# Performance work log

Hardware: AMD Instinct MI355X
Metric: run time of the kernel (lower is better)

Reference implementation:

```python
import jax, jax.numpy as jnp
import numpy as np

B, T, D = 2, 4096, 512
H = 8  # heads; head_dim = D // H = 64


def setup_inputs() -> dict:
    key = jax.random.key(0)
    ks = jax.random.split(key, 8)
    s = 0.02
    return {
        "queries": jax.random.normal(ks[0], (B, T, D), jnp.float32),
        "keys": jax.random.normal(ks[1], (B, T, D), jnp.float32),
        "values": jax.random.normal(ks[2], (B, T, D), jnp.float32),
        "Wq": jax.random.normal(ks[3], (D, D), jnp.float32) * s,
        "Wk": jax.random.normal(ks[4], (D, D), jnp.float32) * s,
        "Wv": jax.random.normal(ks[5], (D, D), jnp.float32) * s,
        "Wo": jax.random.normal(ks[6], (D, D), jnp.float32) * s,
        "bo": jnp.zeros((D,), jnp.float32),
    }


def reference(queries, keys, values, Wq, Wk, Wv, Wo, bo):
    # pad_dim = 0 for in_dim=512, n_heads=8, so no padding needed.
    Bq, Tq, _ = queries.shape
    Ts = keys.shape[1]
    hd = D // H
    # torch Linear: x @ W.T
    q = (queries @ Wq.T).reshape(Bq, Tq, H, hd).transpose(0, 2, 1, 3)  # [B,H,T,hd]
    k = (keys @ Wk.T).reshape(Bq, Ts, H, hd).transpose(0, 2, 1, 3)
    v = (values @ Wv.T).reshape(Bq, Ts, H, hd).transpose(0, 2, 1, 3)
    attn = jnp.einsum("bhtd,bhsd->bhts", q, k) / np.sqrt(hd).astype(np.float32)
    attn = jax.nn.softmax(attn, axis=-1)  # [B,H,T,Ts]
    z = jnp.einsum("bhts,bhsd->bhtd", attn, v)
    z = z.transpose(0, 2, 1, 3).reshape(Bq, Tq, D)
    out = z @ Wo.T + bo
    return (out, attn)
```

## Files before the change

### kernel.cpp

```cpp
#include <hip/hip_runtime.h>

typedef __attribute__((ext_vector_type(8))) short bf16x8;
typedef __attribute__((ext_vector_type(8))) unsigned short u16x8;
typedef __attribute__((ext_vector_type(4))) float f32x4;
typedef __attribute__((ext_vector_type(2))) unsigned uint2v;

#define DEVINL __device__ __forceinline__

constexpr int TB = 2;
constexpr int TT = 4096;
constexpr int TD = 512;
constexpr int TH = 8;
constexpr int THD = 64;
constexpr int TM = TB * TT;

DEVINL unsigned short f2b(float f) {
  unsigned u = __builtin_bit_cast(unsigned, f);
  u += 0x7FFFu + ((u >> 16) & 1u);
  return (unsigned short)(u >> 16);
}

DEVINL unsigned cvtpk(float lo, float hi) {
  unsigned r;
  asm("v_cvt_pk_bf16_f32 %0, %1, %2" : "=v"(r) : "v"(lo), "v"(hi));
  return r;
}

DEVINL void lgkm_barrier() {
  asm volatile("s_waitcnt lgkmcnt(0)" ::: "memory");
  __builtin_amdgcn_s_barrier();
  __builtin_amdgcn_sched_barrier(0);
}

__global__ __launch_bounds__(256, 2)
void proj_qkv(const float* __restrict__ Xq, const float* __restrict__ Xk,
              const float* __restrict__ Xv, const float* __restrict__ Wq,
              const float* __restrict__ Wk, const float* __restrict__ Wv,
              unsigned short* __restrict__ qb, unsigned short* __restrict__ kb,
              unsigned short* __restrict__ vt)
{
  constexpr int K = TD, N = TD;
  __shared__ unsigned short As[128][72];
  __shared__ unsigned short Bs[128][72];

  const int z = blockIdx.z;
  const float* X = (z == 0) ? Xq : (z == 1) ? Xk : Xv;
  const float* W = (z == 0) ? Wq : (z == 1) ? Wk : Wv;
  unsigned short* Yb = (z == 0) ? qb : (z == 1) ? kb : vt;
  const bool TR = (z == 2);

  const int t    = threadIdx.x;
  const int lane = t & 63, w = t >> 6;
  const int fr = lane & 15, fq = lane >> 4;
  const int wr = (w >> 1) * 64, wc = (w & 1) * 64;
  const int bm = blockIdx.x * 128, bn = blockIdx.y * 128;
  const int srow = t >> 1;
  const int skh  = (t & 1) * 32;

  f32x4 acc[4][4];
  #pragma unroll
  for (int i = 0; i < 4; ++i)
    #pragma unroll
    for (int j = 0; j < 4; ++j)
      acc[i][j] = f32x4{0.f, 0.f, 0.f, 0.f};

  for (int k0 = 0; k0 < K; k0 += 64) {
    const float* srcA = X + (size_t)(bm + srow) * K + k0 + skh;
    const float* srcB = W + (size_t)(bn + srow) * K + k0 + skh;
    #pragma unroll
    for (int i = 0; i < 4; ++i) {
      float4 a0 = ((const float4*)srcA)[2 * i];
      float4 a1 = ((const float4*)srcA)[2 * i + 1];
      u16x8 oa = {f2b(a0.x), f2b(a0.y), f2b(a0.z), f2b(a0.w),
                  f2b(a1.x), f2b(a1.y), f2b(a1.z), f2b(a1.w)};
      *(u16x8*)&As[srow][skh + i * 8] = oa;
      float4 b0 = ((const float4*)srcB)[2 * i];
      float4 b1 = ((const float4*)srcB)[2 * i + 1];
      u16x8 ob = {f2b(b0.x), f2b(b0.y), f2b(b0.z), f2b(b0.w),
                  f2b(b1.x), f2b(b1.y), f2b(b1.z), f2b(b1.w)};
      *(u16x8*)&Bs[srow][skh + i * 8] = ob;
    }
    __syncthreads();
    #pragma unroll
    for (int kk = 0; kk < 2; ++kk) {
      bf16x8 af[4], bfv[4];
      #pragma unroll
      for (int i = 0; i < 4; ++i)
        af[i] = *(const bf16x8*)&As[wr + i * 16 + fr][kk * 32 + fq * 8];
      #pragma unroll
      for (int j = 0; j < 4; ++j)
        bfv[j] = *(const bf16x8*)&Bs[wc + j * 16 + fr][kk * 32 + fq * 8];
      if (TR) {
        #pragma unroll
        for (int i = 0; i < 4; ++i)
          #pragma unroll
          for (int j = 0; j < 4; ++j)
            acc[i][j] = __builtin_amdgcn_mfma_f32_16x16x32_bf16(bfv[i], af[j], acc[i][j], 0, 0, 0);
      } else {
        #pragma unroll
        for (int i = 0; i < 4; ++i)
          #pragma unroll
          for (int j = 0; j < 4; ++j)
            acc[i][j] = __builtin_amdgcn_mfma_f32_16x16x32_bf16(af[i], bfv[j], acc[i][j], 0, 0, 0);
      }
    }
    __syncthreads();
  }

  if (TR) {
    #pragma unroll
    for (int i = 0; i < 4; ++i)
      #pragma unroll
      for (int j = 0; j < 4; ++j)
        #pragma unroll
        for (int ii = 0; ii < 4; ++ii) {
          const int Nidx = bn + wc + i * 16 + fq * 4 + ii;
          const int Midx = bm + wr + j * 16 + fr;
          const int h = Nidx >> 6, d = Nidx & (THD - 1);
          const int b = Midx >> 12, tt = Midx & (TT - 1);
          Yb[((size_t)(b * TH + h) * THD + d) * TT + tt] = f2b(acc[i][j][ii]);
        }
  } else {
    #pragma unroll
    for (int i = 0; i < 4; ++i)
      #pragma unroll
      for (int j = 0; j < 4; ++j)
        #pragma unroll
        for (int ii = 0; ii < 4; ++ii) {
          const int gm = bm + wr + i * 16 + fq * 4 + ii;
          const int gn = bn + wc + j * 16 + fr;
          Yb[(size_t)gm * N + gn] = f2b(acc[i][j][ii]);
        }
  }
}

__global__ __launch_bounds__(256, 2)
void gemm_final(const float* __restrict__ X, const float* __restrict__ W,
                float* __restrict__ Yf, const float* __restrict__ bias)
{
  constexpr int K = TD, N = TD;
  __shared__ unsigned short As[128][72];
  __shared__ unsigned short Bs[128][72];

  const int t    = threadIdx.x;
  const int lane = t & 63, w = t >> 6;
  const int fr = lane & 15, fq = lane >> 4;
  const int wr = (w >> 1) * 64, wc = (w & 1) * 64;
  const int bm = blockIdx.x * 128, bn = blockIdx.y * 128;
  const int srow = t >> 1;
  const int skh  = (t & 1) * 32;

  f32x4 acc[4][4];
  #pragma unroll
  for (int i = 0; i < 4; ++i)
    #pragma unroll
    for (int j = 0; j < 4; ++j)
      acc[i][j] = f32x4{0.f, 0.f, 0.f, 0.f};

  for (int k0 = 0; k0 < K; k0 += 64) {
    const float* srcA = X + (size_t)(bm + srow) * K + k0 + skh;
    const float* srcB = W + (size_t)(bn + srow) * K + k0 + skh;
    #pragma unroll
    for (int i = 0; i < 4; ++i) {
      float4 a0 = ((const float4*)srcA)[2 * i];
      float4 a1 = ((const float4*)srcA)[2 * i + 1];
      u16x8 oa = {f2b(a0.x), f2b(a0.y), f2b(a0.z), f2b(a0.w),
                  f2b(a1.x), f2b(a1.y), f2b(a1.z), f2b(a1.w)};
      *(u16x8*)&As[srow][skh + i * 8] = oa;
      float4 b0 = ((const float4*)srcB)[2 * i];
      float4 b1 = ((const float4*)srcB)[2 * i + 1];
      u16x8 ob = {f2b(b0.x), f2b(b0.y), f2b(b0.z), f2b(b0.w),
                  f2b(b1.x), f2b(b1.y), f2b(b1.z), f2b(b1.w)};
      *(u16x8*)&Bs[srow][skh + i * 8] = ob;
    }
    __syncthreads();
    #pragma unroll
    for (int kk = 0; kk < 2; ++kk) {
      bf16x8 af[4], bfv[4];
      #pragma unroll
      for (int i = 0; i < 4; ++i)
        af[i] = *(const bf16x8*)&As[wr + i * 16 + fr][kk * 32 + fq * 8];
      #pragma unroll
      for (int j = 0; j < 4; ++j)
        bfv[j] = *(const bf16x8*)&Bs[wc + j * 16 + fr][kk * 32 + fq * 8];
      #pragma unroll
      for (int i = 0; i < 4; ++i)
        #pragma unroll
        for (int j = 0; j < 4; ++j)
          acc[i][j] = __builtin_amdgcn_mfma_f32_16x16x32_bf16(af[i], bfv[j], acc[i][j], 0, 0, 0);
    }
    __syncthreads();
  }

  #pragma unroll
  for (int i = 0; i < 4; ++i)
    #pragma unroll
    for (int j = 0; j < 4; ++j)
      #pragma unroll
      for (int ii = 0; ii < 4; ++ii) {
        const int gm = bm + wr + i * 16 + fq * 4 + ii;
        const int gn = bn + wc + j * 16 + fr;
        Yf[(size_t)gm * N + gn] = acc[i][j][ii] + bias[gn];
      }
}

__global__ __launch_bounds__(256, 4)
void attn_fused(const unsigned short* __restrict__ Qb,
                const unsigned short* __restrict__ Kb,
                const unsigned short* __restrict__ VTg,
                float* __restrict__ attnO, float* __restrict__ Z)
{
  __shared__ unsigned short Ks[2][32][72];
  __shared__ unsigned short VTs[2][64][40];
  __shared__ unsigned short Ps[4][16][40];

  const int t    = threadIdx.x;
  const int lane = t & 63, w = t >> 6;
  const int fr = lane & 15, fq = lane >> 4;
  const int bh = blockIdx.y;
  const int b  = bh >> 3, h = bh & 7;
  const int q0 = blockIdx.x * 64;

  const size_t rowKV  = ((size_t)(b * TT)) * TD + h * THD;
  const size_t vtBase = (size_t)bh * THD * TT;

  const int trK = t >> 3, tcK = (t & 7) * 8;
  const int trV = t >> 2, tcV = (t & 3) * 8;

  auto loadK = [&](int kv0, u16x8& r) {
    r = *(const u16x8*)(Kb + rowKV + (size_t)(kv0 + trK) * TD + tcK);
  };
  auto loadVT = [&](int kv0, u16x8& r) {
    r = *(const u16x8*)(VTg + vtBase + (size_t)trV * TT + kv0 + tcV);
  };
  auto writeK  = [&](int buf, const u16x8& r) { *(u16x8*)&Ks[buf][trK][tcK]  = r; };
  auto writeVT = [&](int buf, const u16x8& r) { *(u16x8*)&VTs[buf][trV][tcV] = r; };

  const unsigned short* qsrc = Qb + ((size_t)(b * TT + q0 + w * 16 + fr)) * TD + h * THD;
  bf16x8 aq[2];
  aq[0] = *(const bf16x8*)(qsrc + fq * 8);
  aq[1] = *(const bf16x8*)(qsrc + 32 + fq * 8);

  constexpr int KVB = 32;
  constexpr int NT = TT / KVB;
  constexpr float K2 = 0.18033688011112042f;

  u16x8 kr, vr;
  loadK(0, kr);
  writeK(0, kr);
  lgkm_barrier();

  float lsum = 0.f;
  for (int j = 0; j < NT; ++j) {
    const int cur = j & 1;
    if (j + 1 < NT) loadK((j + 1) * KVB, kr);
    __builtin_amdgcn_s_setprio(1);
    #pragma unroll
    for (int n = 0; n < 2; ++n) {
      f32x4 s = f32x4{0.f, 0.f, 0.f, 0.f};
      #pragma unroll
      for (int kk = 0; kk < 2; ++kk) {
        bf16x8 ak = *(const bf16x8*)&Ks[cur][n * 16 + fr][kk * 32 + fq * 8];
        s = __builtin_amdgcn_mfma_f32_16x16x32_bf16(ak, aq[kk], s, 0, 0, 0);
      }
      #pragma unroll
      for (int i = 0; i < 4; ++i)
        lsum += __builtin_amdgcn_exp2f(s[i] * K2);
    }
    __builtin_amdgcn_s_setprio(0);
    if (j + 1 < NT) writeK(cur ^ 1, kr);
    lgkm_barrier();
  }
  lsum += __shfl_xor(lsum, 16, 64);
  lsum += __shfl_xor(lsum, 32, 64);
  const float l2i = -__log2f(lsum);

  loadK(0, kr);
  loadVT(0, vr);
  writeK(0, kr);
  writeVT(0, vr);
  lgkm_barrier();

  f32x4 accz[4];
  #pragma unroll
  for (int n = 0; n < 4; ++n) accz[n] = f32x4{0.f, 0.f, 0.f, 0.f};

  float* arow = attnO + ((size_t)bh * TT + q0 + w * 16 + fr) * TT + fq * 4;

  for (int j = 0; j < NT; ++j) {
    const int cur = j & 1;
    const int kv0 = j * KVB;
    if (j + 1 < NT) {
      loadK((j + 1) * KVB, kr);
      loadVT((j + 1) * KVB, vr);
    }
    f32x4 sv[2];
    __builtin_amdgcn_s_setprio(1);
    #pragma unroll
    for (int n = 0; n < 2; ++n) {
      f32x4 s = f32x4{0.f, 0.f, 0.f, 0.f};
      #pragma unroll
      for (int kk = 0; kk < 2; ++kk) {
        bf16x8 ak = *(const bf16x8*)&Ks[cur][n * 16 + fr][kk * 32 + fq * 8];
        s = __builtin_amdgcn_mfma_f32_16x16x32_bf16(ak, aq[kk], s, 0, 0, 0);
      }
      sv[n] = s;
    }
    __builtin_amdgcn_s_setprio(0);
    #pragma unroll
    for (int n = 0; n < 2; ++n) {
      float p0 = __builtin_amdgcn_exp2f(fmaf(sv[n][0], K2, l2i));
      float p1 = __builtin_amdgcn_exp2f(fmaf(sv[n][1], K2, l2i));
      float p2 = __builtin_amdgcn_exp2f(fmaf(sv[n][2], K2, l2i));
      float p3 = __builtin_amdgcn_exp2f(fmaf(sv[n][3], K2, l2i));
      f32x4 pv4 = {p0, p1, p2, p3};
      *(f32x4*)(arow + kv0 + n * 16) = pv4;
      uint2v u = {cvtpk(p0, p1), cvtpk(p2, p3)};
      *(uint2v*)&Ps[w][fr][n * 16 + fq * 4] = u;
    }
    asm volatile("s_waitcnt lgkmcnt(0)" ::: "memory");
    __builtin_amdgcn_sched_barrier(0);
    __builtin_amdgcn_s_setprio(1);
    {
      bf16x8 ap = *(const bf16x8*)&Ps[w][fr][fq * 8];
      #pragma unroll
      for (int df = 0; df < 4; ++df) {
        bf16x8 bv = *(const bf16x8*)&VTs[cur][df * 16 + fr][fq * 8];
        accz[df] = __builtin_amdgcn_mfma_f32_16x16x32_bf16(ap, bv, accz[df], 0, 0, 0);
      }
    }
    __builtin_amdgcn_s_setprio(0);
    if (j + 1 < NT) {
      writeK(cur ^ 1, kr);
      writeVT(cur ^ 1, vr);
    }
    lgkm_barrier();
  }

  const size_t zbase = ((size_t)(b * TT + q0 + w * 16 + fq * 4)) * TD + h * THD + fr;
  #pragma unroll
  for (int df = 0; df < 4; ++df)
    #pragma unroll
    for (int i = 0; i < 4; ++i)
      Z[zbase + (size_t)i * TD + df * 16] = accz[df][i];
}

extern "C" void kernel_launch(void* const* d_in, const int* in_sizes, int n_in,
                              void* d_out, int out_size, void* d_ws, size_t ws_size,
                              hipStream_t stream) {
  const float* queries = (const float*)d_in[0];
  const float* keys    = (const float*)d_in[1];
  const float* values  = (const float*)d_in[2];
  const float* Wq = (const float*)d_in[3];
  const float* Wk = (const float*)d_in[4];
  const float* Wv = (const float*)d_in[5];
  const float* Wo = (const float*)d_in[6];
  const float* bo = (const float*)d_in[7];

  float* out  = (float*)d_out;
  float* attn = out + (size_t)TM * TD;

  unsigned short* qb = (unsigned short*)d_ws;
  unsigned short* kb = qb + (size_t)TM * TD;
  unsigned short* vt = kb + (size_t)TM * TD;
  float*          zf = (float*)(vt + (size_t)TM * TD);

  proj_qkv<<<dim3(TM / 128, TD / 128, 3), 256, 0, stream>>>(
      queries, keys, values, Wq, Wk, Wv, qb, kb, vt);

  attn_fused<<<dim3(TT / 64, TB * TH), 256, 0, stream>>>(qb, kb, vt, attn, zf);

  gemm_final<<<dim3(TM / 128, TD / 128), 256, 0, stream>>>(zf, Wo, out, bo);
}
```

Measured before the change: 536.9 us.

## Fuse softmax sum into PV pass, keep P in registers, remap blocks

The attention kernel now accumulates the softmax denominator during the P·V pass and normalizes Z at the end, instead of running a separate sum pass first. The P tile is packed straight into MFMA operand registers rather than round-tripping through shared memory. A second QK pass then writes the normalized attention matrix, which is still required output. The grid is flattened to 1D with a head-interleaved block mapping meant to improve K/V cache locality across concurrently running blocks. Without a running max, exp2 of the unshifted scores could overflow for large logits, the same assumption the old sum pass already made.

```diff
diff --git a/kernel.cpp b/kernel.cpp
--- a/kernel.cpp
+++ b/kernel.cpp
@@ -4,6 +4,7 @@
 typedef __attribute__((ext_vector_type(8))) unsigned short u16x8;
 typedef __attribute__((ext_vector_type(4))) float f32x4;
 typedef __attribute__((ext_vector_type(2))) unsigned uint2v;
+typedef __attribute__((ext_vector_type(4))) unsigned uint4v;
 
 #define DEVINL __device__ __forceinline__
 
@@ -116,9 +117,9 @@
         for (int ii = 0; ii < 4; ++ii) {
           const int Nidx = bn + wc + i * 16 + fq * 4 + ii;
           const int Midx = bm + wr + j * 16 + fr;
-          const int h = Nidx >> 6, d = Nidx & (THD - 1);
+          const int h = Nidx >> 6, dd = Nidx & (THD - 1);
           const int b = Midx >> 12, tt = Midx & (TT - 1);
-          Yb[((size_t)(b * TH + h) * THD + d) * TT + tt] = f2b(acc[i][j][ii]);
+          Yb[((size_t)(b * TH + h) * THD + dd) * TT + tt] = f2b(acc[i][j][ii]);
         }
   } else {
     #pragma unroll
@@ -212,14 +213,15 @@
 {
   __shared__ unsigned short Ks[2][32][72];
   __shared__ unsigned short VTs[2][64][40];
-  __shared__ unsigned short Ps[4][16][40];
 
   const int t    = threadIdx.x;
   const int lane = t & 63, w = t >> 6;
   const int fr = lane & 15, fq = lane >> 4;
-  const int bh = blockIdx.y;
+
+  const int d  = blockIdx.x;
+  const int bh = 2 * (d & 7) + ((d >> 3) & 1);
+  const int q0 = (d >> 4) * 64;
   const int b  = bh >> 3, h = bh & 7;
-  const int q0 = blockIdx.x * 64;
 
   const size_t rowKV  = ((size_t)(b * TT)) * TD + h * THD;
   const size_t vtBase = (size_t)bh * THD * TT;
@@ -247,49 +249,18 @@
 
   u16x8 kr, vr;
   loadK(0, kr);
-  writeK(0, kr);
-  lgkm_barrier();
-
-  float lsum = 0.f;
-  for (int j = 0; j < NT; ++j) {
-    const int cur = j & 1;
-    if (j + 1 < NT) loadK((j + 1) * KVB, kr);
-    __builtin_amdgcn_s_setprio(1);
-    #pragma unroll
-    for (int n = 0; n < 2; ++n) {
-      f32x4 s = f32x4{0.f, 0.f, 0.f, 0.f};
-      #pragma unroll
-      for (int kk = 0; kk < 2; ++kk) {
-        bf16x8 ak = *(const bf16x8*)&Ks[cur][n * 16 + fr][kk * 32 + fq * 8];
-        s = __builtin_amdgcn_mfma_f32_16x16x32_bf16(ak, aq[kk], s, 0, 0, 0);
-      }
-      #pragma unroll
-      for (int i = 0; i < 4; ++i)
-        lsum += __builtin_amdgcn_exp2f(s[i] * K2);
-    }
-    __builtin_amdgcn_s_setprio(0);
-    if (j + 1 < NT) writeK(cur ^ 1, kr);
-    lgkm_barrier();
-  }
-  lsum += __shfl_xor(lsum, 16, 64);
-  lsum += __shfl_xor(lsum, 32, 64);
-  const float l2i = -__log2f(lsum);
-
-  loadK(0, kr);
   loadVT(0, vr);
   writeK(0, kr);
   writeVT(0, vr);
   lgkm_barrier();
 
+  float lsum = 0.f;
   f32x4 accz[4];
   #pragma unroll
   for (int n = 0; n < 4; ++n) accz[n] = f32x4{0.f, 0.f, 0.f, 0.f};
-
-  float* arow = attnO + ((size_t)bh * TT + q0 + w * 16 + fr) * TT + fq * 4;
 
   for (int j = 0; j < NT; ++j) {
     const int cur = j & 1;
-    const int kv0 = j * KVB;
     if (j + 1 < NT) {
       loadK((j + 1) * KVB, kr);
       loadVT((j + 1) * KVB, vr);
@@ -307,27 +278,25 @@
       sv[n] = s;
     }
     __builtin_amdgcn_s_setprio(0);
-    #pragma unroll
-    for (int n = 0; n < 2; ++n) {
-      float p0 = __builtin_amdgcn_exp2f(fmaf(sv[n][0], K2, l2i));
-      float p1 = __builtin_amdgcn_exp2f(fmaf(sv[n][1], K2, l2i));
-      float p2 = __builtin_amdgcn_exp2f(fmaf(sv[n][2], K2, l2i));
-      float p3 = __builtin_amdgcn_exp2f(fmaf(sv[n][3], K2, l2i));
-      f32x4 pv4 = {p0, p1, p2, p3};
-      *(f32x4*)(arow + kv0 + n * 16) = pv4;
-      uint2v u = {cvtpk(p0, p1), cvtpk(p2, p3)};
-      *(uint2v*)&Ps[w][fr][n * 16 + fq * 4] = u;
-    }
-    asm volatile("s_waitcnt lgkmcnt(0)" ::: "memory");
-    __builtin_amdgcn_sched_barrier(0);
+    float p[2][4];
+    #pragma unroll
+    for (int n = 0; n < 2; ++n)
+      #pragma unroll
+      for (int i = 0; i < 4; ++i) {
+        p[n][i] = __builtin_amdgcn_exp2f(sv[n][i] * K2);
+        lsum += p[n][i];
+      }
+    uint4v pav = {cvtpk(p[0][0], p[0][1]), cvtpk(p[0][2], p[0][3]),
+                  cvtpk(p[1][0], p[1][1]), cvtpk(p[1][2], p[1][3])};
+    bf16x8 ap = __builtin_bit_cast(bf16x8, pav);
     __builtin_amdgcn_s_setprio(1);
-    {
-      bf16x8 ap = *(const bf16x8*)&Ps[w][fr][fq * 8];
-      #pragma unroll
-      for (int df = 0; df < 4; ++df) {
-        bf16x8 bv = *(const bf16x8*)&VTs[cur][df * 16 + fr][fq * 8];
-        accz[df] = __builtin_amdgcn_mfma_f32_16x16x32_bf16(ap, bv, accz[df], 0, 0, 0);
-      }
+    #pragma unroll
+    for (int df = 0; df < 4; ++df) {
+      uint2v lo = *(const uint2v*)&VTs[cur][df * 16 + fr][fq * 4];
+      uint2v hi = *(const uint2v*)&VTs[cur][df * 16 + fr][16 + fq * 4];
+      uint4v bvv = {lo[0], lo[1], hi[0], hi[1]};
+      accz[df] = __builtin_amdgcn_mfma_f32_16x16x32_bf16(
+          ap, __builtin_bit_cast(bf16x8, bvv), accz[df], 0, 0, 0);
     }
     __builtin_amdgcn_s_setprio(0);
     if (j + 1 < NT) {
@@ -337,12 +306,54 @@
     lgkm_barrier();
   }
 
+  lsum += __shfl_xor(lsum, 16, 64);
+  lsum += __shfl_xor(lsum, 32, 64);
+
+  float rls[4];
+  #pragma unroll
+  for (int i = 0; i < 4; ++i)
+    rls[i] = 1.0f / __shfl(lsum, fq * 4 + i, 64);
   const size_t zbase = ((size_t)(b * TT + q0 + w * 16 + fq * 4)) * TD + h * THD + fr;
   #pragma unroll
   for (int df = 0; df < 4; ++df)
     #pragma unroll
     for (int i = 0; i < 4; ++i)
-      Z[zbase + (size_t)i * TD + df * 16] = accz[df][i];
+      Z[zbase + (size_t)i * TD + df * 16] = accz[df][i] * rls[i];
+
+  const float l2i = -__log2f(lsum);
+  loadK(0, kr);
+  writeK(0, kr);
+  lgkm_barrier();
+
+  float* arow = attnO + ((size_t)bh * TT + q0 + w * 16 + fr) * TT + fq * 4;
+
+  for (int j = 0; j < NT; ++j) {
+    const int cur = j & 1;
+    if (j + 1 < NT) loadK((j + 1) * KVB, kr);
+    f32x4 sv[2];
+    __builtin_amdgcn_s_setprio(1);
+    #pragma unroll
+    for (int n = 0; n < 2; ++n) {
+      f32x4 s = f32x4{0.f, 0.f, 0.f, 0.f};
+      #pragma unroll
+      for (int kk = 0; kk < 2; ++kk) {
+        bf16x8 ak = *(const bf16x8*)&Ks[cur][n * 16 + fr][kk * 32 + fq * 8];
+        s = __builtin_amdgcn_mfma_f32_16x16x32_bf16(ak, aq[kk], s, 0, 0, 0);
+      }
+      sv[n] = s;
+    }
+    __builtin_amdgcn_s_setprio(0);
+    #pragma unroll
+    for (int n = 0; n < 2; ++n) {
+      f32x4 pv4 = {__builtin_amdgcn_exp2f(fmaf(sv[n][0], K2, l2i)),
+                   __builtin_amdgcn_exp2f(fmaf(sv[n][1], K2, l2i)),
+                   __builtin_amdgcn_exp2f(fmaf(sv[n][2], K2, l2i)),
+                   __builtin_amdgcn_exp2f(fmaf(sv[n][3], K2, l2i))};
+      *(f32x4*)(arow + j * KVB + n * 16) = pv4;
+    }
+    if (j + 1 < NT) writeK(cur ^ 1, kr);
+    lgkm_barrier();
+  }
 }
 
 extern "C" void kernel_launch(void* const* d_in, const int* in_sizes, int n_in,
@@ -368,7 +379,7 @@
   proj_qkv<<<dim3(TM / 128, TD / 128, 3), 256, 0, stream>>>(
       queries, keys, values, Wq, Wk, Wv, qb, kb, vt);
 
-  attn_fused<<<dim3(TT / 64, TB * TH), 256, 0, stream>>>(qb, kb, vt, attn, zf);
+  attn_fused<<<dim3(1024), 256, 0, stream>>>(qb, kb, vt, attn, zf);
 
   gemm_final<<<dim3(TM / 128, TD / 128), 256, 0, stream>>>(zf, Wo, out, bo);
 }
```

Result: faster. 521.8 us (-2.8%).
